# Performance work log

Measured on AMD Instinct MI355X. Metric: run time of the kernel, lower is better.

## Reference

```python
import jax, jax.numpy as jnp
import numpy as np

B, S, D, H, DFF, K = 16, 1024, 1024, 16, 4096, 3


def setup_inputs() -> dict:
    key = jax.random.key(0)
    ks = jax.random.split(key, 8)
    f = lambda k, sh: jax.random.normal(k, sh, jnp.float32) * 0.02
    return dict(
        x=jax.random.normal(ks[0], (B, S, D), jnp.float32),
        mask=jnp.ones((B, 1, S), jnp.int32),
        alpha1=jnp.ones((D,), jnp.float32), bias1=jnp.zeros((D,), jnp.float32),
        alpha2=jnp.ones((D,), jnp.float32), bias2=jnp.zeros((D,), jnp.float32),
        W_l1=f(ks[1], (D, 2 * D)), b_l1=jnp.zeros((2 * D,), jnp.float32),
        conv_w=f(ks[2], (H, K)),
        W_l2=f(ks[3], (D, D)), b_l2=jnp.zeros((D,), jnp.float32),
        W_ff1=f(ks[4], (D, DFF)), b_ff1=jnp.zeros((DFF,), jnp.float32),
        W_ff2=f(ks[5], (DFF, D)), b_ff2=jnp.zeros((D,), jnp.float32),
    )


def _norm(x, alpha, bias, eps=1e-6):
    # Norm: alpha * (x - mean) / (std + eps) + bias, torch std is unbiased (ddof=1)
    mu = x.mean(-1, keepdims=True)
    sd = x.std(-1, keepdims=True, ddof=1)
    return alpha * (x - mu) / (sd + eps) + bias


def _lightconv(x, conv_w):
    # x: [B, S, C]; conv_w: [H, K] softmax-normalized over K; channels in a head share kernel
    C = x.shape[-1]
    w = jax.nn.softmax(conv_w, axis=-1)              # [H, K]
    wk = jnp.repeat(w, C // H, axis=0)[:, None, :]   # [C, 1, K] depthwise kernel
    y = jax.lax.conv_general_dilated(
        x.transpose(0, 2, 1), wk, (1,), [(K // 2, (K - 1) // 2)],
        dimension_numbers=('NCH', 'OIH', 'NCH'), feature_group_count=C)
    return y.transpose(0, 2, 1)


def reference(x, mask, alpha1, bias1, alpha2, bias2, W_l1, b_l1, conv_w,
              W_l2, b_l2, W_ff1, b_ff1, W_ff2, b_ff2):
    # --- lightweight-conv sublayer ---
    res = x
    h = _norm(x, alpha1, bias1)
    h = h @ W_l1 + b_l1                         # [B,S,2C]
    a, b = jnp.split(h, 2, axis=-1)
    h = a * jax.nn.sigmoid(b)                   # GLU -> [B,S,C]
    cm = mask[:, -1, :][:, :, None]             # [B,S,1]
    h = jnp.where(cm == 0, 0.0, h)
    h = _lightconv(h, conv_w)
    h = h @ W_l2 + b_l2
    x = res + h
    # --- FFN sublayer ---
    res = x
    h = _norm(x, alpha2, bias2)
    h = jax.nn.relu(h @ W_ff1 + b_ff1) @ W_ff2 + b_ff2
    return res + h
```

## Files before the change

### kernel.cpp

```cpp
#include <hip/hip_runtime.h>

typedef unsigned short ushort_t;
typedef __attribute__((ext_vector_type(8))) short s8v;
typedef __attribute__((ext_vector_type(4))) float f4v;

__device__ __forceinline__ float b2f(ushort_t h) {
    union { unsigned u; float f; } c; c.u = ((unsigned)h) << 16; return c.f;
}
__device__ __forceinline__ ushort_t f2b(float f) {
    union { float f; unsigned u; } c; c.f = f;
    unsigned u = c.u;
    return (ushort_t)((u + 0x7fffu + ((u >> 16) & 1u)) >> 16);
}

__device__ __forceinline__ void glds16(const void* g, void* l) {
    __builtin_amdgcn_global_load_lds(
        (const __attribute__((address_space(1))) void*)g,
        (__attribute__((address_space(3))) void*)l, 16, 0, 0);
}

__global__ __launch_bounds__(256) void trans_k(const float* __restrict__ W,
                                               ushort_t* __restrict__ Wt,
                                               int K, int N) {
    __shared__ float tile[64][65];
    int k0 = blockIdx.x * 64, n0 = blockIdx.y * 64;
    int t = threadIdx.x;
    int c = t & 63, r4 = t >> 6;
#pragma unroll
    for (int i = 0; i < 16; ++i) {
        int r = i * 4 + r4;
        tile[r][c] = W[(size_t)(k0 + r) * N + n0 + c];
    }
    __syncthreads();
#pragma unroll
    for (int i = 0; i < 16; ++i) {
        int r = i * 4 + r4;
        Wt[(size_t)(n0 + r) * K + k0 + c] = f2b(tile[c][r]);
    }
}

__global__ __launch_bounds__(256) void norm_k(const float* __restrict__ x,
                                              const float* __restrict__ al,
                                              const float* __restrict__ be,
                                              ushort_t* __restrict__ out) {
    int row = blockIdx.x;
    const float4* xr = (const float4*)(x + (size_t)row * 1024);
    float4 v = xr[threadIdx.x];
    float s = v.x + v.y + v.z + v.w;
    float q = v.x * v.x + v.y * v.y + v.z * v.z + v.w * v.w;
#pragma unroll
    for (int o = 32; o > 0; o >>= 1) {
        s += __shfl_down(s, o);
        q += __shfl_down(q, o);
    }
    __shared__ float ss[4], qq[4];
    int lane = threadIdx.x & 63, wv = threadIdx.x >> 6;
    if (lane == 0) { ss[wv] = s; qq[wv] = q; }
    __syncthreads();
    s = ss[0] + ss[1] + ss[2] + ss[3];
    q = qq[0] + qq[1] + qq[2] + qq[3];
    float mu = s * (1.f / 1024.f);
    float var = (q - 1024.f * mu * mu) * (1.f / 1023.f);
    var = fmaxf(var, 0.f);
    float inv = 1.f / (sqrtf(var) + 1e-6f);
    float4 a4 = ((const float4*)al)[threadIdx.x];
    float4 b4 = ((const float4*)be)[threadIdx.x];
    ushort4 o4;
    o4.x = f2b(a4.x * (v.x - mu) * inv + b4.x);
    o4.y = f2b(a4.y * (v.y - mu) * inv + b4.y);
    o4.z = f2b(a4.z * (v.z - mu) * inv + b4.z);
    o4.w = f2b(a4.w * (v.w - mu) * inv + b4.w);
    ((ushort4*)(out + (size_t)row * 1024))[threadIdx.x] = o4;
}

__global__ __launch_bounds__(256) void glu_k(const ushort_t* __restrict__ t1,
                                             const int* __restrict__ mask,
                                             ushort_t* __restrict__ g) {
    int i = blockIdx.x * 256 + threadIdx.x;
    int row = i >> 7;
    int cc = (i & 127) << 3;
    int b = row >> 10, s = row & 1023;
    size_t base = (size_t)row * 2048;
    s8v va = *(const s8v*)(t1 + base + cc);
    s8v vb = *(const s8v*)(t1 + base + 1024 + cc);
    float mval = (mask[b * 1024 + s] == 0) ? 0.f : 1.f;
    s8v ov;
#pragma unroll
    for (int j = 0; j < 8; ++j) {
        float a = b2f((ushort_t)va[j]);
        float xx = b2f((ushort_t)vb[j]);
        float sg = 1.f / (1.f + __expf(-xx));
        ov[j] = (short)f2b(a * sg * mval);
    }
    *(s8v*)(g + (size_t)row * 1024 + cc) = ov;
}

__global__ __launch_bounds__(256) void conv_k(const ushort_t* __restrict__ g,
                                              const float* __restrict__ cw,
                                              ushort_t* __restrict__ out) {
    int i = blockIdx.x * 256 + threadIdx.x;
    int row = i >> 7;
    int cc = (i & 127) << 3;
    int s = row & 1023;
    int head = cc >> 6;
    float w0 = cw[head * 3 + 0], w1 = cw[head * 3 + 1], w2 = cw[head * 3 + 2];
    float mx = fmaxf(w0, fmaxf(w1, w2));
    float e0 = __expf(w0 - mx), e1 = __expf(w1 - mx), e2 = __expf(w2 - mx);
    float inv = 1.f / (e0 + e1 + e2);
    w0 = e0 * inv; w1 = e1 * inv; w2 = e2 * inv;
    size_t base = (size_t)row * 1024 + cc;
    s8v z = {0, 0, 0, 0, 0, 0, 0, 0};
    s8v vm = (s > 0)    ? *(const s8v*)(g + base - 1024) : z;
    s8v v0 = *(const s8v*)(g + base);
    s8v vp = (s < 1023) ? *(const s8v*)(g + base + 1024) : z;
    s8v ov;
#pragma unroll
    for (int j = 0; j < 8; ++j) {
        float r = w0 * b2f((ushort_t)vm[j]) + w1 * b2f((ushort_t)v0[j]) +
                  w2 * b2f((ushort_t)vp[j]);
        ov[j] = (short)f2b(r);
    }
    *(s8v*)(out + base) = ov;
}

template <int EPI>
__global__ __launch_bounds__(512, 1) void gemm_k(const ushort_t* __restrict__ A,
                                                 const ushort_t* __restrict__ Bt,
                                                 const float* __restrict__ bias,
                                                 const float* res, float* outf,
                                                 ushort_t* outb, int N, int K) {
    __shared__ char smem[131072] __attribute__((aligned(128)));
    const int NBN = N >> 8;
    const int nwg = gridDim.x;
    const int per = nwg >> 3;
    const int tt = (blockIdx.x & 7) * per + (blockIdx.x >> 3);
    const int gw = NBN << 3;
    const int g = tt / gw;
    const int rem = tt - g * gw;
    const int bm = (g << 3) + (rem & 7);
    const int bn = rem >> 3;

    const int t = threadIdx.x;
    const int l = t & 63, w = t >> 6;
    const int wm = w >> 2, wn = w & 3;
    const int lr = l & 15, lk = l >> 4;

    const int swzel = (((t & 3) ^ ((t >> 3) & 3)) << 3);
    const int r0 = t >> 2;
    const ushort_t* pA0 = A + (size_t)(bm * 256 + r0) * K + swzel;
    const ushort_t* pA1 = pA0 + (size_t)128 * K;
    const ushort_t* pB0 = Bt + (size_t)(bn * 256 + r0) * K + swzel;
    const ushort_t* pB1 = pB0 + (size_t)128 * K;

    const int fswz = ((lk ^ ((lr >> 1) & 3)) << 4);
    int aoff[8], boff[4];
#pragma unroll
    for (int m = 0; m < 8; ++m)
        aoff[m] = (wm * 128 + m * 16 + lr) * 64 + fswz;
#pragma unroll
    for (int n = 0; n < 4; ++n)
        boff[n] = 16384 + (wn * 64 + n * 16 + lr) * 64 + fswz;

    f4v acc[8][4];
#pragma unroll
    for (int m = 0; m < 8; ++m)
#pragma unroll
        for (int n = 0; n < 4; ++n) acc[m][n] = f4v{0.f, 0.f, 0.f, 0.f};

    const int NK = K >> 5;

#pragma unroll
    for (int p = 0; p < 3; ++p) {
        char* d = smem + p * 32768 + t * 16;
        glds16(pA0 + p * 32, d);
        glds16(pA1 + p * 32, d + 8192);
        glds16(pB0 + p * 32, d + 16384);
        glds16(pB1 + p * 32, d + 24576);
    }
    asm volatile("s_waitcnt vmcnt(8)" ::: "memory");
    __builtin_amdgcn_s_barrier();
    __builtin_amdgcn_sched_barrier(0);

    for (int i = 0; i < NK; ++i) {
        const char* cb = smem + (size_t)(i & 3) * 32768;
        int st = i + 3; if (st >= NK) st = NK - 1;
        char* sd = smem + (size_t)((i + 3) & 3) * 32768 + t * 16;
        const int ko = st * 32;

        s8v aL[4], bF[4], aH[4];
#pragma unroll
        for (int m = 0; m < 4; ++m) aL[m] = *(const s8v*)(cb + aoff[m]);
#pragma unroll
        for (int n = 0; n < 4; ++n) bF[n] = *(const s8v*)(cb + boff[n]);
        __builtin_amdgcn_s_barrier();
        __builtin_amdgcn_sched_barrier(0);
        glds16(pA0 + ko, sd);
        glds16(pA1 + ko, sd + 8192);
        __builtin_amdgcn_s_setprio(1);
#pragma unroll
        for (int m = 0; m < 4; ++m)
#pragma unroll
            for (int n = 0; n < 4; ++n)
                acc[m][n] = __builtin_amdgcn_mfma_f32_16x16x32_bf16(
                    aL[m], bF[n], acc[m][n], 0, 0, 0);
        __builtin_amdgcn_s_setprio(0);

#pragma unroll
        for (int m = 0; m < 4; ++m) aH[m] = *(const s8v*)(cb + aoff[4 + m]);
        asm volatile("s_waitcnt vmcnt(6)" ::: "memory");
        __builtin_amdgcn_s_barrier();
        __builtin_amdgcn_sched_barrier(0);
        glds16(pB0 + ko, sd + 16384);
        glds16(pB1 + ko, sd + 24576);
        __builtin_amdgcn_s_setprio(1);
#pragma unroll
        for (int m = 0; m < 4; ++m)
#pragma unroll
            for (int n = 0; n < 4; ++n)
                acc[4 + m][n] = __builtin_amdgcn_mfma_f32_16x16x32_bf16(
                    aH[m], bF[n], acc[4 + m][n], 0, 0, 0);
        __builtin_amdgcn_s_setprio(0);
    }

    if (EPI == 1) {
#pragma unroll
        for (int n = 0; n < 4; ++n) {
            int gcol = bn * 256 + wn * 64 + n * 16 + lr;
            float bb = bias[gcol];
#pragma unroll
            for (int m = 0; m < 8; ++m) {
#pragma unroll
                for (int r = 0; r < 4; ++r) {
                    int grow = bm * 256 + wm * 128 + m * 16 + lk * 4 + r;
                    size_t oi = (size_t)grow * N + gcol;
                    outf[oi] = acc[m][n][r] + bb + res[oi];
                }
            }
        }
    } else {
        asm volatile("s_waitcnt vmcnt(0)" ::: "memory");
        __builtin_amdgcn_s_barrier();
        float bb4[4];
#pragma unroll
        for (int n = 0; n < 4; ++n)
            bb4[n] = bias[bn * 256 + wn * 64 + n * 16 + lr];
#pragma unroll
        for (int m = 0; m < 8; ++m)
#pragma unroll
            for (int n = 0; n < 4; ++n)
#pragma unroll
                for (int r = 0; r < 4; ++r) {
                    int row = wm * 128 + m * 16 + lk * 4 + r;
                    int colb = ((wn * 64 + n * 16 + lr) * 2) ^ ((row & 3) << 4);
                    float v = acc[m][n][r] + bb4[n];
                    if (EPI == 2) v = fmaxf(v, 0.f);
                    *(ushort_t*)(smem + row * 512 + colb) = f2b(v);
                }
        __builtin_amdgcn_s_barrier();
#pragma unroll
        for (int s = 0; s < 16; ++s) {
            int row = s * 16 + (t >> 5);
            int byt = row * 512 + (((t & 31) * 16) ^ ((row & 3) << 4));
            int grow = bm * 256 + row;
            int gcol = bn * 256 + (t & 31) * 8;
            *(s8v*)(outb + (size_t)grow * N + gcol) = *(const s8v*)(smem + byt);
        }
    }
}

extern "C" void kernel_launch(void* const* d_in, const int* in_sizes, int n_in,
                              void* d_out, int out_size, void* d_ws, size_t ws_size,
                              hipStream_t stream) {
    const float* x      = (const float*)d_in[0];
    const int*   mask   = (const int*)d_in[1];
    const float* alpha1 = (const float*)d_in[2];
    const float* bias1  = (const float*)d_in[3];
    const float* alpha2 = (const float*)d_in[4];
    const float* bias2  = (const float*)d_in[5];
    const float* W_l1   = (const float*)d_in[6];
    const float* b_l1   = (const float*)d_in[7];
    const float* conv_w = (const float*)d_in[8];
    const float* W_l2   = (const float*)d_in[9];
    const float* b_l2   = (const float*)d_in[10];
    const float* W_ff1  = (const float*)d_in[11];
    const float* b_ff1  = (const float*)d_in[12];
    const float* W_ff2  = (const float*)d_in[13];
    const float* b_ff2  = (const float*)d_in[14];
    float* out = (float*)d_out;

    char* ws = (char*)d_ws;
    size_t off = 0;
    auto alloc = [&](size_t b) {
        char* p = ws + off;
        off += (b + 255) & ~(size_t)255;
        return p;
    };
    ushort_t* Wl1t  = (ushort_t*)alloc(2048ull * 1024 * 2);
    ushort_t* Wl2t  = (ushort_t*)alloc(1024ull * 1024 * 2);
    ushort_t* Wff1t = (ushort_t*)alloc(4096ull * 1024 * 2);
    ushort_t* Wff2t = (ushort_t*)alloc(1024ull * 4096 * 2);
    char* regA = alloc(134217728ull);
    ushort_t* B1 = (ushort_t*)alloc(33554432ull);
    ushort_t* C1 = (ushort_t*)alloc(33554432ull);
    ushort_t* t1 = (ushort_t*)regA;
    ushort_t* f1 = (ushort_t*)regA;

    const int R = 16384;

    trans_k<<<dim3(16, 32), 256, 0, stream>>>(W_l1, Wl1t, 1024, 2048);
    trans_k<<<dim3(16, 16), 256, 0, stream>>>(W_l2, Wl2t, 1024, 1024);
    trans_k<<<dim3(16, 64), 256, 0, stream>>>(W_ff1, Wff1t, 1024, 4096);
    trans_k<<<dim3(64, 16), 256, 0, stream>>>(W_ff2, Wff2t, 4096, 1024);

    norm_k<<<R, 256, 0, stream>>>(x, alpha1, bias1, B1);
    gemm_k<0><<<64 * 8, 512, 0, stream>>>(B1, Wl1t, b_l1, nullptr, nullptr, t1, 2048, 1024);
    glu_k<<<8192, 256, 0, stream>>>(t1, mask, B1);
    conv_k<<<8192, 256, 0, stream>>>(B1, conv_w, C1);
    gemm_k<1><<<64 * 4, 512, 0, stream>>>(C1, Wl2t, b_l2, x, out, nullptr, 1024, 1024);

    norm_k<<<R, 256, 0, stream>>>(out, alpha2, bias2, B1);
    gemm_k<2><<<64 * 16, 512, 0, stream>>>(B1, Wff1t, b_ff1, nullptr, nullptr, f1, 4096, 1024);
    gemm_k<1><<<64 * 4, 512, 0, stream>>>(f1, Wff2t, b_ff2, out, out, nullptr, 1024, 4096);
}
```

Baseline: 576.2 us.

## Restructure GEMM main loop to double-buffered 64-wide K stages with four phases

Replaces the 4-deep ring of 32-wide K buffers with two 64 KB buffers, each holding a 64-wide K slab. Each iteration runs four MFMA phases, and the global-to-LDS loads for the next slab are interleaved between them, guarded by extra barriers and explicit lgkmcnt/vmcnt waits. The aim is to halve loop trips and per-iteration overhead while keeping loads overlapped with compute. The trade-off is shallower prefetch depth and more barriers per iteration, which can expose memory latency.

Result: no change. 577.3 us (+0.2%).

```diff
diff --git a/kernel.cpp b/kernel.cpp
--- a/kernel.cpp
+++ b/kernel.cpp
@@ -159,7 +159,7 @@
         aoff[m] = (wm * 128 + m * 16 + lr) * 64 + fswz;
 #pragma unroll
     for (int n = 0; n < 4; ++n)
-        boff[n] = 16384 + (wn * 64 + n * 16 + lr) * 64 + fswz;
+        boff[n] = 32768 + (wn * 64 + n * 16 + lr) * 64 + fswz;
 
     f4v acc[8][4];
 #pragma unroll
@@ -167,60 +167,113 @@
 #pragma unroll
         for (int n = 0; n < 4; ++n) acc[m][n] = f4v{0.f, 0.f, 0.f, 0.f};
 
-    const int NK = K >> 5;
-
-#pragma unroll
-    for (int p = 0; p < 3; ++p) {
-        char* d = smem + p * 32768 + t * 16;
-        glds16(pA0 + p * 32, d);
-        glds16(pA1 + p * 32, d + 8192);
-        glds16(pB0 + p * 32, d + 16384);
-        glds16(pB1 + p * 32, d + 24576);
-    }
-    asm volatile("s_waitcnt vmcnt(8)" ::: "memory");
+    const int NK = K >> 6;
+
+    glds16(pA0 + 0, smem + t * 16);
+    glds16(pA1 + 0, smem + 8192 + t * 16);
+    glds16(pB0 + 0, smem + 32768 + t * 16);
+    glds16(pB1 + 0, smem + 40960 + t * 16);
+    glds16(pA0 + 32, smem + 16384 + t * 16);
+    glds16(pA1 + 32, smem + 24576 + t * 16);
+    glds16(pB0 + 32, smem + 49152 + t * 16);
+    glds16(pB1 + 32, smem + 57344 + t * 16);
+    asm volatile("s_waitcnt vmcnt(4)");
     __builtin_amdgcn_s_barrier();
-    __builtin_amdgcn_sched_barrier(0);
 
     for (int i = 0; i < NK; ++i) {
-        const char* cb = smem + (size_t)(i & 3) * 32768;
-        int st = i + 3; if (st >= NK) st = NK - 1;
-        char* sd = smem + (size_t)((i + 3) & 3) * 32768 + t * 16;
-        const int ko = st * 32;
-
-        s8v aL[4], bF[4], aH[4];
-#pragma unroll
-        for (int m = 0; m < 4; ++m) aL[m] = *(const s8v*)(cb + aoff[m]);
-#pragma unroll
-        for (int n = 0; n < 4; ++n) bF[n] = *(const s8v*)(cb + boff[n]);
-        __builtin_amdgcn_s_barrier();
-        __builtin_amdgcn_sched_barrier(0);
-        glds16(pA0 + ko, sd);
-        glds16(pA1 + ko, sd + 8192);
+        const char* cb = smem + (size_t)(i & 1) * 65536;
+        char* sb = (char*)smem + (size_t)((i + 1) & 1) * 65536;
+        const int nx = (i + 1 < NK ? i + 1 : NK - 1) * 64;
+        s8v bF0[4], bF1[4], aF[4];
+
+        __builtin_amdgcn_sched_barrier(0);
+#pragma unroll
+        for (int n = 0; n < 4; ++n) bF0[n] = *(const s8v*)(cb + boff[n]);
+#pragma unroll
+        for (int m = 0; m < 4; ++m) aF[m] = *(const s8v*)(cb + aoff[m]);
+        glds16(pA0 + nx, sb + t * 16);
+        glds16(pA1 + nx, sb + 8192 + t * 16);
+        __builtin_amdgcn_sched_barrier(0);
+        __builtin_amdgcn_s_barrier();
+        asm volatile("s_waitcnt lgkmcnt(0)");
+        __builtin_amdgcn_sched_barrier(0);
         __builtin_amdgcn_s_setprio(1);
 #pragma unroll
         for (int m = 0; m < 4; ++m)
 #pragma unroll
             for (int n = 0; n < 4; ++n)
                 acc[m][n] = __builtin_amdgcn_mfma_f32_16x16x32_bf16(
-                    aL[m], bF[n], acc[m][n], 0, 0, 0);
+                    aF[m], bF0[n], acc[m][n], 0, 0, 0);
         __builtin_amdgcn_s_setprio(0);
-
-#pragma unroll
-        for (int m = 0; m < 4; ++m) aH[m] = *(const s8v*)(cb + aoff[4 + m]);
-        asm volatile("s_waitcnt vmcnt(6)" ::: "memory");
-        __builtin_amdgcn_s_barrier();
-        __builtin_amdgcn_sched_barrier(0);
-        glds16(pB0 + ko, sd + 16384);
-        glds16(pB1 + ko, sd + 24576);
+        __builtin_amdgcn_s_barrier();
+
+        __builtin_amdgcn_sched_barrier(0);
+#pragma unroll
+        for (int m = 0; m < 4; ++m) aF[m] = *(const s8v*)(cb + aoff[4 + m]);
+        glds16(pB0 + nx, sb + 32768 + t * 16);
+        glds16(pB1 + nx, sb + 40960 + t * 16);
+        asm volatile("s_waitcnt vmcnt(4)");
+        __builtin_amdgcn_sched_barrier(0);
+        __builtin_amdgcn_s_barrier();
+        asm volatile("s_waitcnt lgkmcnt(0)");
+        __builtin_amdgcn_sched_barrier(0);
         __builtin_amdgcn_s_setprio(1);
 #pragma unroll
         for (int m = 0; m < 4; ++m)
 #pragma unroll
             for (int n = 0; n < 4; ++n)
                 acc[4 + m][n] = __builtin_amdgcn_mfma_f32_16x16x32_bf16(
-                    aH[m], bF[n], acc[4 + m][n], 0, 0, 0);
+                    aF[m], bF0[n], acc[4 + m][n], 0, 0, 0);
         __builtin_amdgcn_s_setprio(0);
-    }
+        __builtin_amdgcn_s_barrier();
+
+        __builtin_amdgcn_sched_barrier(0);
+#pragma unroll
+        for (int n = 0; n < 4; ++n)
+            bF1[n] = *(const s8v*)(cb + 16384 + boff[n]);
+#pragma unroll
+        for (int m = 0; m < 4; ++m)
+            aF[m] = *(const s8v*)(cb + 16384 + aoff[m]);
+        glds16(pA0 + nx + 32, sb + 16384 + t * 16);
+        glds16(pA1 + nx + 32, sb + 24576 + t * 16);
+        __builtin_amdgcn_sched_barrier(0);
+        __builtin_amdgcn_s_barrier();
+        asm volatile("s_waitcnt lgkmcnt(0)");
+        __builtin_amdgcn_sched_barrier(0);
+        __builtin_amdgcn_s_setprio(1);
+#pragma unroll
+        for (int m = 0; m < 4; ++m)
+#pragma unroll
+            for (int n = 0; n < 4; ++n)
+                acc[m][n] = __builtin_amdgcn_mfma_f32_16x16x32_bf16(
+                    aF[m], bF1[n], acc[m][n], 0, 0, 0);
+        __builtin_amdgcn_s_setprio(0);
+        __builtin_amdgcn_s_barrier();
+
+        __builtin_amdgcn_sched_barrier(0);
+#pragma unroll
+        for (int m = 0; m < 4; ++m)
+            aF[m] = *(const s8v*)(cb + 16384 + aoff[4 + m]);
+        glds16(pB0 + nx + 32, sb + 49152 + t * 16);
+        glds16(pB1 + nx + 32, sb + 57344 + t * 16);
+        asm volatile("s_waitcnt vmcnt(4)");
+        __builtin_amdgcn_sched_barrier(0);
+        __builtin_amdgcn_s_barrier();
+        asm volatile("s_waitcnt lgkmcnt(0)");
+        __builtin_amdgcn_sched_barrier(0);
+        __builtin_amdgcn_s_setprio(1);
+#pragma unroll
+        for (int m = 0; m < 4; ++m)
+#pragma unroll
+            for (int n = 0; n < 4; ++n)
+                acc[4 + m][n] = __builtin_amdgcn_mfma_f32_16x16x32_bf16(
+                    aF[m], bF1[n], acc[4 + m][n], 0, 0, 0);
+        __builtin_amdgcn_s_setprio(0);
+        __builtin_amdgcn_s_barrier();
+    }
+
+    asm volatile("s_waitcnt vmcnt(0)");
+    __builtin_amdgcn_s_barrier();
 
     if (EPI == 1) {
 #pragma unroll
@@ -238,8 +291,6 @@
             }
         }
     } else {
-        asm volatile("s_waitcnt vmcnt(0)" ::: "memory");
-        __builtin_amdgcn_s_barrier();
         float bb4[4];
 #pragma unroll
         for (int n = 0; n < 4; ++n)
```

## Shrink GEMM tile to 128x256 with 3-stage pipeline and fuse GLU with conv

Applied to the files above, without the earlier changes.

The GEMM tile is reduced from 256x256 to 128x256, with a 3-stage LDS ring buffer of 72KB and one barrier per k-step. This lets multiple workgroups share a CU, and the tile swizzle grouping is widened. The GLU and depthwise conv are fused into one kernel that recomputes the gated activations for the three taps, which removes an intermediate tensor write and read. The trade-off is lower per-tile data reuse, more global traffic for B, and redundant sigmoid computation.

New measurement: 613.1 us. 1.06x slower.

```diff
diff --git a/kernel.cpp b/kernel.cpp
--- a/kernel.cpp
+++ b/kernel.cpp
@@ -73,72 +73,59 @@
     ((ushort4*)(out + (size_t)row * 1024))[threadIdx.x] = o4;
 }
 
-__global__ __launch_bounds__(256) void glu_k(const ushort_t* __restrict__ t1,
-                                             const int* __restrict__ mask,
-                                             ushort_t* __restrict__ g) {
+__global__ __launch_bounds__(256) void gluconv_k(const ushort_t* __restrict__ t1,
+                                                 const int* __restrict__ mask,
+                                                 const float* __restrict__ cw,
+                                                 ushort_t* __restrict__ out) {
     int i = blockIdx.x * 256 + threadIdx.x;
     int row = i >> 7;
     int cc = (i & 127) << 3;
     int b = row >> 10, s = row & 1023;
-    size_t base = (size_t)row * 2048;
-    s8v va = *(const s8v*)(t1 + base + cc);
-    s8v vb = *(const s8v*)(t1 + base + 1024 + cc);
-    float mval = (mask[b * 1024 + s] == 0) ? 0.f : 1.f;
-    s8v ov;
-#pragma unroll
-    for (int j = 0; j < 8; ++j) {
-        float a = b2f((ushort_t)va[j]);
-        float xx = b2f((ushort_t)vb[j]);
-        float sg = 1.f / (1.f + __expf(-xx));
-        ov[j] = (short)f2b(a * sg * mval);
-    }
-    *(s8v*)(g + (size_t)row * 1024 + cc) = ov;
-}
-
-__global__ __launch_bounds__(256) void conv_k(const ushort_t* __restrict__ g,
-                                              const float* __restrict__ cw,
-                                              ushort_t* __restrict__ out) {
-    int i = blockIdx.x * 256 + threadIdx.x;
-    int row = i >> 7;
-    int cc = (i & 127) << 3;
-    int s = row & 1023;
     int head = cc >> 6;
     float w0 = cw[head * 3 + 0], w1 = cw[head * 3 + 1], w2 = cw[head * 3 + 2];
     float mx = fmaxf(w0, fmaxf(w1, w2));
     float e0 = __expf(w0 - mx), e1 = __expf(w1 - mx), e2 = __expf(w2 - mx);
     float inv = 1.f / (e0 + e1 + e2);
-    w0 = e0 * inv; w1 = e1 * inv; w2 = e2 * inv;
-    size_t base = (size_t)row * 1024 + cc;
-    s8v z = {0, 0, 0, 0, 0, 0, 0, 0};
-    s8v vm = (s > 0)    ? *(const s8v*)(g + base - 1024) : z;
-    s8v v0 = *(const s8v*)(g + base);
-    s8v vp = (s < 1023) ? *(const s8v*)(g + base + 1024) : z;
+    float wt[3] = {e0 * inv, e1 * inv, e2 * inv};
+    float a8[8] = {0.f, 0.f, 0.f, 0.f, 0.f, 0.f, 0.f, 0.f};
+#pragma unroll
+    for (int tap = 0; tap < 3; ++tap) {
+        int ss = s + tap - 1;
+        if (ss < 0 || ss > 1023) continue;
+        float wm = (mask[b * 1024 + ss] == 0) ? 0.f : wt[tap];
+        size_t base = (size_t)(row + tap - 1) * 2048 + cc;
+        s8v va = *(const s8v*)(t1 + base);
+        s8v vb = *(const s8v*)(t1 + base + 1024);
+#pragma unroll
+        for (int j = 0; j < 8; ++j) {
+            float a = b2f((ushort_t)va[j]);
+            float xx = b2f((ushort_t)vb[j]);
+            float sg = 1.f / (1.f + __expf(-xx));
+            a8[j] += wm * a * sg;
+        }
+    }
     s8v ov;
 #pragma unroll
-    for (int j = 0; j < 8; ++j) {
-        float r = w0 * b2f((ushort_t)vm[j]) + w1 * b2f((ushort_t)v0[j]) +
-                  w2 * b2f((ushort_t)vp[j]);
-        ov[j] = (short)f2b(r);
-    }
-    *(s8v*)(out + base) = ov;
+    for (int j = 0; j < 8; ++j) ov[j] = (short)f2b(a8[j]);
+    *(s8v*)(out + (size_t)row * 1024 + cc) = ov;
 }
 
 template <int EPI>
-__global__ __launch_bounds__(512, 1) void gemm_k(const ushort_t* __restrict__ A,
+__global__ __launch_bounds__(512, 4) void gemm_k(const ushort_t* __restrict__ A,
                                                  const ushort_t* __restrict__ Bt,
                                                  const float* __restrict__ bias,
                                                  const float* res, float* outf,
                                                  ushort_t* outb, int N, int K) {
-    __shared__ char smem[131072] __attribute__((aligned(128)));
+    __shared__ char smem[73728] __attribute__((aligned(128)));
     const int NBN = N >> 8;
     const int nwg = gridDim.x;
     const int per = nwg >> 3;
     const int tt = (blockIdx.x & 7) * per + (blockIdx.x >> 3);
-    const int gw = NBN << 3;
+    const int gw = NBN << 4;
     const int g = tt / gw;
     const int rem = tt - g * gw;
-    const int bm = (g << 3) + (rem & 7);
-    const int bn = rem >> 3;
+    const int bm = (g << 4) + (rem & 15);
+    const int bn = rem >> 4;
 
     const int t = threadIdx.x;
     const int l = t & 63, w = t >> 6;
@@ -147,80 +134,78 @@
 
     const int swzel = (((t & 3) ^ ((t >> 3) & 3)) << 3);
     const int r0 = t >> 2;
-    const ushort_t* pA0 = A + (size_t)(bm * 256 + r0) * K + swzel;
-    const ushort_t* pA1 = pA0 + (size_t)128 * K;
+    const ushort_t* pA0 = A + (size_t)(bm * 128 + r0) * K + swzel;
     const ushort_t* pB0 = Bt + (size_t)(bn * 256 + r0) * K + swzel;
     const ushort_t* pB1 = pB0 + (size_t)128 * K;
 
     const int fswz = ((lk ^ ((lr >> 1) & 3)) << 4);
-    int aoff[8], boff[4];
-#pragma unroll
-    for (int m = 0; m < 8; ++m)
-        aoff[m] = (wm * 128 + m * 16 + lr) * 64 + fswz;
+    int aoff[4], boff[4];
+#pragma unroll
+    for (int m = 0; m < 4; ++m)
+        aoff[m] = (wm * 64 + m * 16 + lr) * 64 + fswz;
 #pragma unroll
     for (int n = 0; n < 4; ++n)
-        boff[n] = 16384 + (wn * 64 + n * 16 + lr) * 64 + fswz;
-
-    f4v acc[8][4];
-#pragma unroll
-    for (int m = 0; m < 8; ++m)
+        boff[n] = 8192 + (wn * 64 + n * 16 + lr) * 64 + fswz;
+
+    f4v acc[4][4];
+#pragma unroll
+    for (int m = 0; m < 4; ++m)
 #pragma unroll
         for (int n = 0; n < 4; ++n) acc[m][n] = f4v{0.f, 0.f, 0.f, 0.f};
 
     const int NK = K >> 5;
 
-#pragma unroll
-    for (int p = 0; p < 3; ++p) {
-        char* d = smem + p * 32768 + t * 16;
-        glds16(pA0 + p * 32, d);
-        glds16(pA1 + p * 32, d + 8192);
-        glds16(pB0 + p * 32, d + 16384);
-        glds16(pB1 + p * 32, d + 24576);
-    }
-    asm volatile("s_waitcnt vmcnt(8)" ::: "memory");
+    {
+        char* d0 = smem + t * 16;
+        glds16(pA0 + 0, d0);
+        glds16(pB0 + 0, d0 + 8192);
+        glds16(pB1 + 0, d0 + 16384);
+        char* d1 = smem + 24576 + t * 16;
+        glds16(pA0 + 32, d1);
+        glds16(pB0 + 32, d1 + 8192);
+        glds16(pB1 + 32, d1 + 16384);
+    }
+    asm volatile("s_waitcnt vmcnt(3)");
     __builtin_amdgcn_s_barrier();
     __builtin_amdgcn_sched_barrier(0);
 
+    int cur = 0;
     for (int i = 0; i < NK; ++i) {
-        const char* cb = smem + (size_t)(i & 3) * 32768;
-        int st = i + 3; if (st >= NK) st = NK - 1;
-        char* sd = smem + (size_t)((i + 3) & 3) * 32768 + t * 16;
+        const char* cb = smem + cur;
+        int nx2 = cur + 49152; if (nx2 >= 73728) nx2 -= 73728;
+        int st = i + 2; if (st >= NK) st = NK - 1;
         const int ko = st * 32;
-
-        s8v aL[4], bF[4], aH[4];
-#pragma unroll
-        for (int m = 0; m < 4; ++m) aL[m] = *(const s8v*)(cb + aoff[m]);
+        char* sd = smem + nx2 + t * 16;
+
+        glds16(pA0 + ko, sd);
+        glds16(pB0 + ko, sd + 8192);
+        glds16(pB1 + ko, sd + 16384);
+
+        s8v aF[4], bF[4];
+#pragma unroll
+        for (int m = 0; m < 4; ++m) aF[m] = *(const s8v*)(cb + aoff[m]);
 #pragma unroll
         for (int n = 0; n < 4; ++n) bF[n] = *(const s8v*)(cb + boff[n]);
+        __builtin_amdgcn_s_setprio(1);
+#pragma unroll
+        for (int m = 0; m < 4; ++m)
+#pragma unroll
+            for (int n = 0; n < 4; ++n)
+                acc[m][n] = __builtin_amdgcn_mfma_f32_16x16x32_bf16(
+                    aF[m], bF[n], acc[m][n], 0, 0, 0);
+        __builtin_amdgcn_s_setprio(0);
+
+        __builtin_amdgcn_sched_barrier(0);
+        asm volatile("s_waitcnt lgkmcnt(0)");
+        asm volatile("s_waitcnt vmcnt(3)");
         __builtin_amdgcn_s_barrier();
         __builtin_amdgcn_sched_barrier(0);
-        glds16(pA0 + ko, sd);
-        glds16(pA1 + ko, sd + 8192);
-        __builtin_amdgcn_s_setprio(1);
-#pragma unroll
-        for (int m = 0; m < 4; ++m)
-#pragma unroll
-            for (int n = 0; n < 4; ++n)
-                acc[m][n] = __builtin_amdgcn_mfma_f32_16x16x32_bf16(
-                    aL[m], bF[n], acc[m][n], 0, 0, 0);
-        __builtin_amdgcn_s_setprio(0);
-
-#pragma unroll
-        for (int m = 0; m < 4; ++m) aH[m] = *(const s8v*)(cb + aoff[4 + m]);
-        asm volatile("s_waitcnt vmcnt(6)" ::: "memory");
-        __builtin_amdgcn_s_barrier();
-        __builtin_amdgcn_sched_barrier(0);
-        glds16(pB0 + ko, sd + 16384);
-        glds16(pB1 + ko, sd + 24576);
-        __builtin_amdgcn_s_setprio(1);
-#pragma unroll
-        for (int m = 0; m < 4; ++m)
-#pragma unroll
-            for (int n = 0; n < 4; ++n)
-                acc[4 + m][n] = __builtin_amdgcn_mfma_f32_16x16x32_bf16(
-                    aH[m], bF[n], acc[4 + m][n], 0, 0, 0);
-        __builtin_amdgcn_s_setprio(0);
-    }
+
+        cur += 24576; if (cur >= 73728) cur = 0;
+    }
+
+    asm volatile("s_waitcnt vmcnt(0)");
+    __builtin_amdgcn_s_barrier();
 
     if (EPI == 1) {
 #pragma unroll
@@ -228,29 +213,27 @@
             int gcol = bn * 256 + wn * 64 + n * 16 + lr;
             float bb = bias[gcol];
 #pragma unroll
-            for (int m = 0; m < 8; ++m) {
+            for (int m = 0; m < 4; ++m) {
 #pragma unroll
                 for (int r = 0; r < 4; ++r) {
-                    int grow = bm * 256 + wm * 128 + m * 16 + lk * 4 + r;
+                    int grow = bm * 128 + wm * 64 + m * 16 + lk * 4 + r;
                     size_t oi = (size_t)grow * N + gcol;
                     outf[oi] = acc[m][n][r] + bb + res[oi];
                 }
             }
         }
     } else {
-        asm volatile("s_waitcnt vmcnt(0)" ::: "memory");
-        __builtin_amdgcn_s_barrier();
         float bb4[4];
 #pragma unroll
         for (int n = 0; n < 4; ++n)
             bb4[n] = bias[bn * 256 + wn * 64 + n * 16 + lr];
 #pragma unroll
-        for (int m = 0; m < 8; ++m)
+        for (int m = 0; m < 4; ++m)
 #pragma unroll
             for (int n = 0; n < 4; ++n)
 #pragma unroll
                 for (int r = 0; r < 4; ++r) {
-                    int row = wm * 128 + m * 16 + lk * 4 + r;
+                    int row = wm * 64 + m * 16 + lk * 4 + r;
                     int colb = ((wn * 64 + n * 16 + lr) * 2) ^ ((row & 3) << 4);
                     float v = acc[m][n][r] + bb4[n];
                     if (EPI == 2) v = fmaxf(v, 0.f);
@@ -258,10 +241,10 @@
                 }
         __builtin_amdgcn_s_barrier();
 #pragma unroll
-        for (int s = 0; s < 16; ++s) {
+        for (int s = 0; s < 8; ++s) {
             int row = s * 16 + (t >> 5);
             int byt = row * 512 + (((t & 31) * 16) ^ ((row & 3) << 4));
-            int grow = bm * 256 + row;
+            int grow = bm * 128 + row;
             int gcol = bn * 256 + (t & 31) * 8;
             *(s8v*)(outb + (size_t)grow * N + gcol) = *(const s8v*)(smem + byt);
         }
@@ -313,12 +296,11 @@
     trans_k<<<dim3(64, 16), 256, 0, stream>>>(W_ff2, Wff2t, 4096, 1024);
 
     norm_k<<<R, 256, 0, stream>>>(x, alpha1, bias1, B1);
-    gemm_k<0><<<64 * 8, 512, 0, stream>>>(B1, Wl1t, b_l1, nullptr, nullptr, t1, 2048, 1024);
-    glu_k<<<8192, 256, 0, stream>>>(t1, mask, B1);
-    conv_k<<<8192, 256, 0, stream>>>(B1, conv_w, C1);
-    gemm_k<1><<<64 * 4, 512, 0, stream>>>(C1, Wl2t, b_l2, x, out, nullptr, 1024, 1024);
+    gemm_k<0><<<128 * 8, 512, 0, stream>>>(B1, Wl1t, b_l1, nullptr, nullptr, t1, 2048, 1024);
+    gluconv_k<<<8192, 256, 0, stream>>>(t1, mask, conv_w, C1);
+    gemm_k<1><<<128 * 4, 512, 0, stream>>>(C1, Wl2t, b_l2, x, out, nullptr, 1024, 1024);
 
     norm_k<<<R, 256, 0, stream>>>(out, alpha2, bias2, B1);
-    gemm_k<2><<<64 * 16, 512, 0, stream>>>(B1, Wff1t, b_ff1, nullptr, nullptr, f1, 4096, 1024);
-    gemm_k<1><<<64 * 4, 512, 0, stream>>>(f1, Wff2t, b_ff2, out, out, nullptr, 1024, 4096);
-}
+    gemm_k<2><<<128 * 16, 512, 0, stream>>>(B1, Wff1t, b_ff1, nullptr, nullptr, f1, 4096, 1024);
+    gemm_k<1><<<128 * 4, 512, 0, stream>>>(f1, Wff2t, b_ff2, out, out, nullptr, 1024, 4096);
+}
```
